# Performance work log

Hardware: AMD Instinct MI355X
Metric: run time of the kernel (lower is better)

The kernel has to match this reference:

```python
import jax, jax.numpy as jnp
import numpy as np

NEG_BIG = -1e10


def setup_inputs() -> dict:
    key = jax.random.key(0)
    k1, k2, k3 = jax.random.split(key, 3)
    B, C, S, H = 4, 32, 64, 256
    inputs = jax.random.normal(k1, (B, C, S, H), dtype=jnp.float32)
    mask = jnp.ones((B, C, S), dtype=jnp.float32)
    att_self = jax.random.uniform(k2, (B, C, S), dtype=jnp.float32)
    W = jax.random.normal(k3, (H, H), dtype=jnp.float32) * (1.0 / np.sqrt(H))
    return {"inputs": inputs, "mask": mask, "att_self": att_self, "W": W}


def reference(inputs, mask, att_self, W):
    # inputs: [B, C, S, H]; mask, att_self: [B, C, S]; W: [H, H] (linear1, no bias)
    # linear1(inputs2): x @ W^T applied to the query-side copy
    proj = jnp.einsum('bish,gh->bisg', inputs, W)          # [B, C, S, H]
    # scores[b,i,j,s,t] = proj[b,i,s,:] . inputs[b,j,t,:]
    scores = jnp.einsum('bish,bjth->bijst', proj, inputs)  # [B, C, C, S, S]
    # additive mask depends on (j, t) only (key side), broadcast over i and s
    scores = scores + (1.0 - mask)[:, None, :, None, :] * NEG_BIG
    # torch code computes softmax then overwrites with sigmoid -> sigmoid is effective
    att = jax.nn.sigmoid(scores)                            # [B, C, C, S, S]
    ctx = jnp.einsum('bijst,bjth->bijsh', att, inputs)      # [B, C, C, S, H]
    # selfatt weights over s (query sentence tokens), indexed by i
    fused = jnp.einsum('bis,bijsh->bijh', att_self, ctx)    # [B, C, C, H]
    return (fused, att)
```

## Files before the change

kernel.cpp:

```cpp
#include <hip/hip_runtime.h>
#include <hip/hip_bf16.h>

typedef __bf16 bf16x8 __attribute__((ext_vector_type(8)));
typedef float  f32x4  __attribute__((ext_vector_type(4)));

#define NEG_BIG (-1e10f)

constexpr int FUSED_N = 4 * 32 * 32 * 256;


__device__ __forceinline__ void async_ld16(const void* g, void* l) {
    __builtin_amdgcn_global_load_lds(
        (const __attribute__((address_space(1))) void*)g,
        (__attribute__((address_space(3))) void*)l, 16, 0, 0);
}

__device__ __forceinline__ int swzp(int row, int g) {
    return (row * 32 + (g ^ row)) * 8;
}

__global__ __launch_bounds__(256) void convw_kernel(
    const float* __restrict__ W, __bf16* __restrict__ Wh, __bf16* __restrict__ Wl) {
    int idx = blockIdx.x * 256 + threadIdx.x;
    float4 v = ((const float4*)W)[idx];
    float f[4] = {v.x, v.y, v.z, v.w};
    union { __bf16 b[4]; uint2 u; } H, L;
#pragma unroll
    for (int k = 0; k < 4; ++k) {
        __bf16 h = (__bf16)f[k];
        H.b[k] = h;
        L.b[k] = (__bf16)(f[k] - (float)h);
    }
    *(uint2*)&Wh[idx * 4] = H.u;
    *(uint2*)&Wl[idx * 4] = L.u;
}

__global__ __launch_bounds__(256, 2) void prep_kernel(
    const float* __restrict__ Xf,
    const __bf16* __restrict__ Wh, const __bf16* __restrict__ Wl,
    __bf16* __restrict__ XhG, __bf16* __restrict__ XlG,
    __bf16* __restrict__ Ph, __bf16* __restrict__ Pl) {
    __shared__ __align__(16) __bf16 sXh[16 * 256];
    __shared__ __align__(16) __bf16 sXl[16 * 256];
    const int tid = threadIdx.x, rb = blockIdx.x;

#pragma unroll
    for (int it = 0; it < 2; ++it) {
        int idx = it * 256 + tid;
        int row = idx >> 5, g = idx & 31;
        const float* p = Xf + (rb * 16 + row) * 256 + g * 8;
        float4 v0 = *(const float4*)p;
        float4 v1 = *(const float4*)(p + 4);
        float f[8] = {v0.x, v0.y, v0.z, v0.w, v1.x, v1.y, v1.z, v1.w};
        union { __bf16 b[8]; uint4 u; } H, L;
#pragma unroll
        for (int k = 0; k < 8; ++k) {
            __bf16 h = (__bf16)f[k];
            H.b[k] = h;
            L.b[k] = (__bf16)(f[k] - (float)h);
        }
        int go = (rb * 16 + row) * 256 + g * 8;
        *(uint4*)&XhG[go] = H.u;
        *(uint4*)&XlG[go] = L.u;
        int o = swzp(row, g);
        *(uint4*)&sXh[o] = H.u;
        *(uint4*)&sXl[o] = L.u;
    }
    __syncthreads();

    const int lane = tid & 63, wave = tid >> 6, m = lane & 15, quad = lane >> 4;
    bf16x8 Ah[8], Al[8];
#pragma unroll
    for (int k0 = 0; k0 < 8; ++k0) {
        int o = swzp(m, k0 * 4 + quad);
        Ah[k0] = *(const bf16x8*)&sXh[o];
        Al[k0] = *(const bf16x8*)&sXl[o];
    }
    f32x4 acc[4];
    const f32x4 z = {0.f, 0.f, 0.f, 0.f};
#pragma unroll
    for (int n = 0; n < 4; ++n) acc[n] = z;
#pragma unroll
    for (int k0 = 0; k0 < 8; ++k0) {
#pragma unroll
        for (int n = 0; n < 4; ++n) {
            const int gcol = wave * 64 + n * 16 + m;
            const int wo = gcol * 256 + k0 * 32 + quad * 8;
            bf16x8 bh = *(const bf16x8*)&Wh[wo];
            bf16x8 bl = *(const bf16x8*)&Wl[wo];
            acc[n] = __builtin_amdgcn_mfma_f32_16x16x32_bf16(Ah[k0], bh, acc[n], 0, 0, 0);
            acc[n] = __builtin_amdgcn_mfma_f32_16x16x32_bf16(Ah[k0], bl, acc[n], 0, 0, 0);
            acc[n] = __builtin_amdgcn_mfma_f32_16x16x32_bf16(Al[k0], bh, acc[n], 0, 0, 0);
        }
    }
#pragma unroll
    for (int n = 0; n < 4; ++n)
#pragma unroll
        for (int r = 0; r < 4; ++r) {
            int row = rb * 16 + quad * 4 + r;
            int col = wave * 64 + n * 16 + m;
            float v = acc[n][r];
            __bf16 h = (__bf16)v;
            Ph[row * 256 + col] = h;
            Pl[row * 256 + col] = (__bf16)(v - (float)h);
        }
}

__global__ __launch_bounds__(512, 2) void main_kernel(
    const float* __restrict__ Xf, const float* __restrict__ maskf,
    const float* __restrict__ aselff,
    const __bf16* __restrict__ XhG, const __bf16* __restrict__ XlG,
    const __bf16* __restrict__ PhG, const __bf16* __restrict__ PlG,
    float* __restrict__ out) {
    __shared__ __align__(16) __bf16 sPh[64 * 256];
    __shared__ __align__(16) __bf16 sPl[64 * 256];
    __shared__ float sW[8][64];
    const int tid = threadIdx.x;
    const int jq = blockIdx.x & 3;
    const int i  = (blockIdx.x >> 2) & 31;
    const int b  = blockIdx.x >> 7;
    const int lane = tid & 63, wave = tid >> 6, m = lane & 15, quad = lane >> 4;

    const int pbase = (b * 32 + i) * 16384;
    {
        const int rowhalf = lane >> 5;
        const int gslot = lane & 31;
#pragma unroll
        for (int it = 0; it < 4; ++it) {
            const int insti = wave * 4 + it;
            const int row = insti * 2 + rowhalf;
            const int g = gslot ^ (row & 15);
            const int src = pbase + row * 256 + g * 8;
            async_ld16(&PhG[src], &sPh[insti * 512]);
            async_ld16(&PlG[src], &sPl[insti * 512]);
        }
    }

    const float* ap = aselff + (b * 32 + i) * 64;
    float4 asv[4];
#pragma unroll
    for (int rg = 0; rg < 4; ++rg)
        asv[rg] = *(const float4*)&ap[rg * 16 + quad * 4];

    __syncthreads();

    const int j = jq * 8 + wave;
    const int xb = (b * 32 + j) * 16384;

    f32x4 acc[4][4];
    const f32x4 z = {0.f, 0.f, 0.f, 0.f};
#pragma unroll
    for (int rg = 0; rg < 4; ++rg)
#pragma unroll
        for (int ng = 0; ng < 4; ++ng) acc[rg][ng] = z;

#pragma unroll
    for (int k0 = 0; k0 < 8; ++k0) {
        bf16x8 Bh[4], Bl[4];
#pragma unroll
        for (int ng = 0; ng < 4; ++ng) {
            const int bo = xb + (ng * 16 + m) * 256 + k0 * 32 + quad * 8;
            Bh[ng] = *(const bf16x8*)&XhG[bo];
            Bl[ng] = *(const bf16x8*)&XlG[bo];
        }
        bf16x8 Ahk[4], Alk[4];
#pragma unroll
        for (int rg = 0; rg < 4; ++rg) {
            const int o = (rg * 16 + m) * 256 + (((k0 * 4 + quad) ^ m)) * 8;
            Ahk[rg] = *(const bf16x8*)&sPh[o];
            Alk[rg] = *(const bf16x8*)&sPl[o];
        }
#pragma unroll
        for (int rg = 0; rg < 4; ++rg)
#pragma unroll
            for (int ng = 0; ng < 4; ++ng) {
                acc[rg][ng] = __builtin_amdgcn_mfma_f32_16x16x32_bf16(Ahk[rg], Bh[ng], acc[rg][ng], 0, 0, 0);
                acc[rg][ng] = __builtin_amdgcn_mfma_f32_16x16x32_bf16(Ahk[rg], Bl[ng], acc[rg][ng], 0, 0, 0);
                acc[rg][ng] = __builtin_amdgcn_mfma_f32_16x16x32_bf16(Alk[rg], Bh[ng], acc[rg][ng], 0, 0, 0);
            }
    }

    const float* mrow = maskf + (b * 32 + j) * 64;
    float madd[4];
#pragma unroll
    for (int ng = 0; ng < 4; ++ng)
        madd[ng] = (1.0f - mrow[ng * 16 + m]) * NEG_BIG;

    float part[4] = {0.f, 0.f, 0.f, 0.f};
    float* outA = out + FUSED_N + ((size_t)((b * 32 + i) * 32 + j)) * 4096;
#pragma unroll
    for (int rg = 0; rg < 4; ++rg)
#pragma unroll
        for (int r = 0; r < 4; ++r) {
            const int s = rg * 16 + quad * 4 + r;
            const float as_ = ((const float*)&asv[rg])[r];
#pragma unroll
            for (int ng = 0; ng < 4; ++ng) {
                float x = acc[rg][ng][r] + madd[ng];
                float a = 1.0f / (1.0f + __expf(-x));
                outA[s * 64 + ng * 16 + m] = a;
                part[ng] += as_ * a;
            }
        }
#pragma unroll
    for (int ng = 0; ng < 4; ++ng) {
        part[ng] += __shfl_xor(part[ng], 16, 64);
        part[ng] += __shfl_xor(part[ng], 32, 64);
    }
    if (quad == 0) {
#pragma unroll
        for (int ng = 0; ng < 4; ++ng) sW[wave][ng * 16 + m] = part[ng];
    }
    const float* Xg = Xf + xb;
    float4 acf = {0.f, 0.f, 0.f, 0.f};
#pragma unroll 8
    for (int t = 0; t < 64; ++t) {
        const float wv = sW[wave][t];
        float4 xv = *(const float4*)&Xg[t * 256 + lane * 4];
        acf.x += wv * xv.x;
        acf.y += wv * xv.y;
        acf.z += wv * xv.z;
        acf.w += wv * xv.w;
    }
    *(float4*)&out[((size_t)((b * 32 + i) * 32 + j)) * 256 + lane * 4] = acf;
}

extern "C" void kernel_launch(void* const* d_in, const int* in_sizes, int n_in,
                              void* d_out, int out_size, void* d_ws, size_t ws_size,
                              hipStream_t stream) {
    const float* X     = (const float*)d_in[0];
    const float* mask  = (const float*)d_in[1];
    const float* aself = (const float*)d_in[2];
    const float* W     = (const float*)d_in[3];
    float* out = (float*)d_out;

    __bf16* ws = (__bf16*)d_ws;
    const size_t NX = 2097152, NW = 65536;
    __bf16* Xh = ws;
    __bf16* Xl = Xh + NX;
    __bf16* Ph = Xl + NX;
    __bf16* Pl = Ph + NX;
    __bf16* Wh = Pl + NX;
    __bf16* Wl = Wh + NW;

    convw_kernel<<<dim3(64), dim3(256), 0, stream>>>(W, Wh, Wl);
    prep_kernel<<<dim3(512), dim3(256), 0, stream>>>(X, Wh, Wl, Xh, Xl, Ph, Pl);
    main_kernel<<<dim3(512), dim3(512), 0, stream>>>(
        X, mask, aself, Xh, Xl, Ph, Pl, out);
}
```

Baseline: 151.7 us.

## Split query rows across wave pairs and double main kernel grid

Each block now handles 4 key chunks j instead of 8. Its 8 waves split the 64 query rows into two halves, so the grid doubles to 1024 blocks and each wave holds half the accumulators. Partial self-attention weights from the two halves are combined through shared memory after an extra barrier. This is meant to raise parallelism and cut register pressure. The cost is that each block loads the P tile for half as many j, which doubles P traffic and the async loads into LDS, and the X B-fragments are now read twice.

```diff
diff --git a/kernel.cpp b/kernel.cpp
--- a/kernel.cpp
+++ b/kernel.cpp
@@ -115,10 +115,11 @@
     __shared__ __align__(16) __bf16 sPh[64 * 256];
     __shared__ __align__(16) __bf16 sPl[64 * 256];
     __shared__ float sW[8][64];
+    __shared__ float sAs[64];
     const int tid = threadIdx.x;
-    const int jq = blockIdx.x & 3;
-    const int i  = (blockIdx.x >> 2) & 31;
-    const int b  = blockIdx.x >> 7;
+    const int jh = blockIdx.x & 7;
+    const int i  = (blockIdx.x >> 3) & 31;
+    const int b  = blockIdx.x >> 8;
     const int lane = tid & 63, wave = tid >> 6, m = lane & 15, quad = lane >> 4;
 
     const int pbase = (b * 32 + i) * 16384;
@@ -136,21 +137,18 @@
         }
     }
 
-    const float* ap = aselff + (b * 32 + i) * 64;
-    float4 asv[4];
-#pragma unroll
-    for (int rg = 0; rg < 4; ++rg)
-        asv[rg] = *(const float4*)&ap[rg * 16 + quad * 4];
+    if (tid < 64) sAs[tid] = aselff[(b * 32 + i) * 64 + tid];
 
     __syncthreads();
 
-    const int j = jq * 8 + wave;
+    const int jw = wave & 3, sh = wave >> 2;
+    const int j  = jh * 4 + jw;
     const int xb = (b * 32 + j) * 16384;
 
-    f32x4 acc[4][4];
+    f32x4 acc[2][4];
     const f32x4 z = {0.f, 0.f, 0.f, 0.f};
 #pragma unroll
-    for (int rg = 0; rg < 4; ++rg)
+    for (int rg = 0; rg < 2; ++rg)
 #pragma unroll
         for (int ng = 0; ng < 4; ++ng) acc[rg][ng] = z;
 
@@ -163,15 +161,16 @@
             Bh[ng] = *(const bf16x8*)&XhG[bo];
             Bl[ng] = *(const bf16x8*)&XlG[bo];
         }
-        bf16x8 Ahk[4], Alk[4];
-#pragma unroll
-        for (int rg = 0; rg < 4; ++rg) {
-            const int o = (rg * 16 + m) * 256 + (((k0 * 4 + quad) ^ m)) * 8;
+        bf16x8 Ahk[2], Alk[2];
+#pragma unroll
+        for (int rg = 0; rg < 2; ++rg) {
+            const int row = sh * 32 + rg * 16 + m;
+            const int o = row * 256 + (((k0 * 4 + quad) ^ m)) * 8;
             Ahk[rg] = *(const bf16x8*)&sPh[o];
             Alk[rg] = *(const bf16x8*)&sPl[o];
         }
 #pragma unroll
-        for (int rg = 0; rg < 4; ++rg)
+        for (int rg = 0; rg < 2; ++rg)
 #pragma unroll
             for (int ng = 0; ng < 4; ++ng) {
                 acc[rg][ng] = __builtin_amdgcn_mfma_f32_16x16x32_bf16(Ahk[rg], Bh[ng], acc[rg][ng], 0, 0, 0);
@@ -189,11 +188,11 @@
     float part[4] = {0.f, 0.f, 0.f, 0.f};
     float* outA = out + FUSED_N + ((size_t)((b * 32 + i) * 32 + j)) * 4096;
 #pragma unroll
-    for (int rg = 0; rg < 4; ++rg)
+    for (int rg = 0; rg < 2; ++rg)
 #pragma unroll
         for (int r = 0; r < 4; ++r) {
-            const int s = rg * 16 + quad * 4 + r;
-            const float as_ = ((const float*)&asv[rg])[r];
+            const int s = sh * 32 + rg * 16 + quad * 4 + r;
+            const float as_ = sAs[s];
 #pragma unroll
             for (int ng = 0; ng < 4; ++ng) {
                 float x = acc[rg][ng][r] + madd[ng];
@@ -211,18 +210,21 @@
 #pragma unroll
         for (int ng = 0; ng < 4; ++ng) sW[wave][ng * 16 + m] = part[ng];
     }
+
+    __syncthreads();
+
     const float* Xg = Xf + xb;
-    float4 acf = {0.f, 0.f, 0.f, 0.f};
+    const int hbase = sh * 128 + lane * 2;
+    float a0 = 0.f, a1 = 0.f;
 #pragma unroll 8
     for (int t = 0; t < 64; ++t) {
-        const float wv = sW[wave][t];
-        float4 xv = *(const float4*)&Xg[t * 256 + lane * 4];
-        acf.x += wv * xv.x;
-        acf.y += wv * xv.y;
-        acf.z += wv * xv.z;
-        acf.w += wv * xv.w;
-    }
-    *(float4*)&out[((size_t)((b * 32 + i) * 32 + j)) * 256 + lane * 4] = acf;
+        const float wv = sW[jw][t] + sW[jw + 4][t];
+        const float2 xv = *(const float2*)&Xg[t * 256 + hbase];
+        a0 += wv * xv.x;
+        a1 += wv * xv.y;
+    }
+    float2 res = {a0, a1};
+    *(float2*)&out[((size_t)((b * 32 + i) * 32 + j)) * 256 + hbase] = res;
 }
 
 extern "C" void kernel_launch(void* const* d_in, const int* in_sizes, int n_in,
@@ -245,6 +247,6 @@
 
     convw_kernel<<<dim3(64), dim3(256), 0, stream>>>(W, Wh, Wl);
     prep_kernel<<<dim3(512), dim3(256), 0, stream>>>(X, Wh, Wl, Xh, Xl, Ph, Pl);
-    main_kernel<<<dim3(512), dim3(512), 0, stream>>>(
+    main_kernel<<<dim3(1024), dim3(512), 0, stream>>>(
         X, mask, aself, Xh, Xl, Ph, Pl, out);
 }
```

New measurement: 182.1 us. +20.0%, slower.
